# Performance work log

Measured on AMD Instinct MI355X. Metric: run time of the kernel, lower is better.

## Reference

```python
import jax, jax.numpy as jnp
import numpy as np

# ViT-Base config
C, H, W = 3, 224, 224
NP = 14            # n_patches per side
PS = 16            # patch size (H // NP)
IN_D = C * PS * PS # 768
D = 768            # hidden_d
NH = 12            # n_heads
DH = D // NH       # 64
L = 12             # n_blocks
MLP = 4 * D        # mlp_ratio * hidden_d
OUT = 1000         # out_d
B = 64             # batch
S = NP * NP + 1    # 197 tokens (cls + patches)
EPS = 1e-5


def _pos_embed(seq_len, d):
    # get_positional_embeddings: sin on even dims, cos on odd dims
    i = jnp.arange(seq_len, dtype=jnp.float32)[:, None]
    j = jnp.arange(d, dtype=jnp.float32)[None, :]
    angle = i / jnp.power(10000.0, (j - j % 2) / d)
    return jnp.where(j % 2 == 0, jnp.sin(angle), jnp.cos(angle))


def _ln(x, g, b):
    m = x.mean(-1, keepdims=True)
    v = ((x - m) ** 2).mean(-1, keepdims=True)
    return (x - m) * jax.lax.rsqrt(v + EPS) * g + b


def _attn(x, qkv_w, qkv_b, out_w, out_b):
    n, s, _ = x.shape
    qkv = (x @ qkv_w + qkv_b).reshape(n, s, NH, 3, DH)  # matches torch chunk layout
    q, k, v = qkv[..., 0, :], qkv[..., 1, :], qkv[..., 2, :]
    scores = jnp.einsum('bqhd,bkhd->bhqk', q, k) / (DH ** 0.5)
    w = jax.nn.softmax(scores, axis=-1)
    o = jnp.einsum('bhqk,bkhd->bqhd', w, v).reshape(n, s, D)
    return o @ out_w + out_b


def setup_inputs() -> dict:
    key = jax.random.key(0)
    ks = jax.random.split(key, 16)
    sd = 0.02
    return {
        'images': jax.random.normal(ks[0], (B, C, H, W), jnp.float32),
        'lm_w': jax.random.normal(ks[1], (IN_D, D), jnp.float32) * sd,
        'lm_b': jnp.zeros((D,), jnp.float32),
        'cls_tok': jax.random.uniform(ks[2], (1, D), jnp.float32),
        'ln1_g': jnp.ones((L, D), jnp.float32),
        'ln1_b': jnp.zeros((L, D), jnp.float32),
        'qkv_w': jax.random.normal(ks[3], (L, D, 3 * D), jnp.float32) * sd,
        'qkv_b': jnp.zeros((L, 3 * D), jnp.float32),
        'out_w': jax.random.normal(ks[4], (L, D, D), jnp.float32) * sd,
        'out_b': jnp.zeros((L, D), jnp.float32),
        'ln2_g': jnp.ones((L, D), jnp.float32),
        'ln2_b': jnp.zeros((L, D), jnp.float32),
        'mlp1_w': jax.random.normal(ks[5], (L, D, MLP), jnp.float32) * sd,
        'mlp1_b': jnp.zeros((L, MLP), jnp.float32),
        'mlp2_w': jax.random.normal(ks[6], (L, MLP, D), jnp.float32) * sd,
        'mlp2_b': jnp.zeros((L, D), jnp.float32),
        'head_w': jax.random.normal(ks[7], (D, OUT), jnp.float32) * sd,
        'head_b': jnp.zeros((OUT,), jnp.float32),
    }


def reference(images, lm_w, lm_b, cls_tok, ln1_g, ln1_b, qkv_w, qkv_b,
              out_w, out_b, ln2_g, ln2_b, mlp1_w, mlp1_b, mlp2_w, mlp2_b,
              head_w, head_b):
    n = images.shape[0]
    # patchify: (N,C,H,W) -> (N, NP*NP, C*PS*PS), per-patch flatten order (C, ph, pw)
    p = images.reshape(n, C, NP, PS, NP, PS).transpose(0, 2, 4, 1, 3, 5)
    p = p.reshape(n, NP * NP, IN_D)
    tok = p @ lm_w + lm_b                                   # (N, 196, D)
    cls = jnp.broadcast_to(cls_tok, (n, 1, D))
    x = jnp.concatenate([cls, tok], axis=1) + _pos_embed(S, D)
    for l in range(L):
        x = x + _attn(_ln(x, ln1_g[l], ln1_b[l]), qkv_w[l], qkv_b[l], out_w[l], out_b[l])
        h = _ln(x, ln2_g[l], ln2_b[l])
        x = x + (jax.nn.gelu(h @ mlp1_w[l] + mlp1_b[l], approximate=False) @ mlp2_w[l] + mlp2_b[l])
    return jax.nn.softmax(x[:, 0] @ head_w + head_b, axis=-1)
```

## Files before the change

### kernel.cpp

```cpp
#include <hip/hip_runtime.h>
#include <hip/hip_bf16.h>
#include <math.h>

#define WS_B 64
#define WS_S 197
#define WS_D 768
#define WS_NH 12
#define WS_L 12
#define WS_MLP 3072
#define WS_OUT 1000
#define WS_IND 768
#define WS_NPAT 196
#define SP 208
#define JP 224

typedef __attribute__((ext_vector_type(8))) short bf16x8;
typedef __attribute__((ext_vector_type(4))) float f32x4;

static __device__ __forceinline__ float bf2f(short s) {
    unsigned u = ((unsigned)(unsigned short)s) << 16;
    return __builtin_bit_cast(float, u);
}
static __device__ __forceinline__ short f2bf(float f) {
    unsigned u = __builtin_bit_cast(unsigned, f);
    u = (u + 0x7FFF + ((u >> 16) & 1)) >> 16;
    return (short)u;
}

__global__ __launch_bounds__(256) void wconv_kernel(
    const float* __restrict__ W, short* __restrict__ Wh, int K, int N)
{
    int idx = blockIdx.x * 256 + threadIdx.x;
    int total = (K >> 3) * N;
    if (idx >= total) return;
    int n = idx % N, k8 = idx / N, k0 = k8 << 3;
    short hi[8];
#pragma unroll
    for (int j = 0; j < 8; ++j) hi[j] = f2bf(W[(size_t)(k0 + j) * N + n]);
    *(bf16x8*)(Wh + (size_t)n * K + k0) = *(bf16x8*)hi;
}

__global__ __launch_bounds__(256) void mfma_gemm(
    const short* __restrict__ A, int lda,
    const short* __restrict__ Bh,
    const float* __restrict__ bias, const float* __restrict__ res,
    float* __restrict__ outF, short* __restrict__ outH, int ldc,
    int M, int N, int K, int act)
{
    __shared__ short As[128 * 64];
    __shared__ short Bs[128 * 64];

    const int tid = threadIdx.x;
    const int w = tid >> 6, lane = tid & 63;
    const int bm = blockIdx.y * 128, bn = blockIdx.x * 128;
    const int wm = (w >> 1) * 64, wn = (w & 1) * 64;
    const int lr = lane & 15, lq = lane >> 4;

    f32x4 acc[4][4];
#pragma unroll
    for (int i = 0; i < 4; ++i)
#pragma unroll
        for (int j = 0; j < 4; ++j) acc[i][j] = (f32x4){0.f, 0.f, 0.f, 0.f};

    int aoff[2][4], boff[2][4];
#pragma unroll
    for (int ks = 0; ks < 2; ++ks)
#pragma unroll
        for (int f = 0; f < 4; ++f) {
            int r = wm + f * 16 + lr;
            aoff[ks][f] = r * 64 + (((ks * 4 + lq) ^ (lr & 7)) << 3);
            int rn = wn + f * 16 + lr;
            boff[ks][f] = rn * 64 + (((ks * 4 + lq) ^ (lr & 7)) << 3);
        }

    int srow[4], scs[4];
#pragma unroll
    for (int i = 0; i < 4; ++i) {
        int chunk = w * 64 + i * 256 + lane;
        int row = chunk >> 3, c = chunk & 7;
        srow[i] = row;
        scs[i] = c ^ (row & 7);
    }

    for (int k0 = 0; k0 < K; k0 += 64) {
#pragma unroll
        for (int i = 0; i < 4; ++i) {
            int ldsbase = (w * 64 + i * 256) * 8;
            int arow = bm + srow[i]; if (arow >= M) arow = M - 1;
            const short* ga = A + (size_t)arow * lda + k0 + scs[i] * 8;
            __builtin_amdgcn_global_load_lds(
                (const __attribute__((address_space(1))) void*)ga,
                (__attribute__((address_space(3))) void*)(As + ldsbase), 16, 0, 0);
            const short* gh = Bh + (size_t)(bn + srow[i]) * K + k0 + scs[i] * 8;
            __builtin_amdgcn_global_load_lds(
                (const __attribute__((address_space(1))) void*)gh,
                (__attribute__((address_space(3))) void*)(Bs + ldsbase), 16, 0, 0);
        }
        asm volatile("s_waitcnt vmcnt(0)" ::: "memory");
        __syncthreads();

#pragma unroll
        for (int ks = 0; ks < 2; ++ks) {
            bf16x8 av[4], bv[4];
#pragma unroll
            for (int f = 0; f < 4; ++f) av[f] = *(const bf16x8*)&As[aoff[ks][f]];
#pragma unroll
            for (int f = 0; f < 4; ++f) bv[f] = *(const bf16x8*)&Bs[boff[ks][f]];
#pragma unroll
            for (int fm = 0; fm < 4; ++fm)
#pragma unroll
                for (int fn = 0; fn < 4; ++fn)
                    acc[fm][fn] = __builtin_amdgcn_mfma_f32_16x16x32_bf16(
                        av[fm], bv[fn], acc[fm][fn], 0, 0, 0);
        }
        __syncthreads();
    }

#pragma unroll
    for (int fm = 0; fm < 4; ++fm)
#pragma unroll
        for (int fn = 0; fn < 4; ++fn) {
            int gc = bn + wn + fn * 16 + lr;
            float bvs = bias ? bias[gc] : 0.f;
            int grb = bm + wm + fm * 16 + lq * 4;
#pragma unroll
            for (int r = 0; r < 4; ++r) {
                int gr = grb + r;
                if (gr >= M) continue;
                float v = acc[fm][fn][r] + bvs;
                if (act == 1) v = 0.5f * v * (1.f + erff(v * 0.70710678118654752440f));
                if (res) v += res[(size_t)gr * ldc + gc];
                if (outF) outF[(size_t)gr * ldc + gc] = v;
                else      outH[(size_t)gr * ldc + gc] = f2bf(v);
            }
        }
}

__global__ __launch_bounds__(256) void attn_kernel(
    const short* __restrict__ qkv, short* __restrict__ o)
{
    __shared__ short Qs[SP * 64];
    __shared__ short Ks[SP * 64];
    __shared__ short Vt[64 * 256];
    __shared__ short Ps[4][16 * 256];

    const int bh = blockIdx.x;
    const int n = bh / WS_NH, h = bh % WS_NH;
    const short* base = qkv + (size_t)n * WS_S * 2304 + h * 192;
    const int tid = threadIdx.x;
    const int w = tid >> 6, lane = tid & 63;
    const int lr = lane & 15, lq = lane >> 4;

    const bf16x8 z8 = {0, 0, 0, 0, 0, 0, 0, 0};
    for (int i = lane; i < 512; i += 64) *(bf16x8*)&Ps[w][i * 8] = z8;

    for (int u = tid; u < SP * 8; u += 256) {
        int row = u >> 3, c = u & 7;
        int cs = c ^ (row & 7);
        bf16x8 vq = z8, vk = z8;
        if (row < WS_S) {
            const short* rp = base + (size_t)row * 2304;
            vq = *(const bf16x8*)(rp + cs * 8);
            vk = *(const bf16x8*)(rp + 64 + cs * 8);
        }
        *(bf16x8*)&Qs[row * 64 + c * 8] = vq;
        *(bf16x8*)&Ks[row * 64 + c * 8] = vk;
    }

    for (int u = tid; u < 64 * (JP / 2); u += 256) {
        int d = u & 63, jp = u >> 6;
        int j = jp * 2;
        unsigned val = 0;
        if (j < WS_S) {
            unsigned lo = (unsigned short)base[(size_t)j * 2304 + 128 + d];
            unsigned hi = (j + 1 < WS_S) ? (unsigned short)base[(size_t)(j + 1) * 2304 + 128 + d] : 0u;
            val = lo | (hi << 16);
        }
        int cj = j >> 3, e = j & 7;
        *(unsigned*)&Vt[d * 256 + ((cj ^ (d & 7)) << 3) + e] = val;
    }
    __syncthreads();

    for (int qt = w; qt < 13; qt += 4) {
        bf16x8 qv[2];
#pragma unroll
        for (int ks = 0; ks < 2; ++ks)
            qv[ks] = *(const bf16x8*)&Qs[(qt * 16 + lr) * 64 + (((ks * 4 + lq) ^ (lr & 7)) << 3)];
        f32x4 acc[13];
#pragma unroll
        for (int jt = 0; jt < 13; ++jt) acc[jt] = (f32x4){0.f, 0.f, 0.f, 0.f};
#pragma unroll
        for (int jt = 0; jt < 13; ++jt)
#pragma unroll
            for (int ks = 0; ks < 2; ++ks) {
                bf16x8 kv = *(const bf16x8*)&Ks[(jt * 16 + lr) * 64 + (((ks * 4 + lq) ^ (lr & 7)) << 3)];
                acc[jt] = __builtin_amdgcn_mfma_f32_16x16x32_bf16(kv, qv[ks], acc[jt], 0, 0, 0);
            }

        float s[13][4];
        float m = -1e30f;
#pragma unroll
        for (int jt = 0; jt < 13; ++jt)
#pragma unroll
            for (int r = 0; r < 4; ++r) {
                int j = jt * 16 + lq * 4 + r;
                float v = acc[jt][r] * 0.125f;
                s[jt][r] = v;
                if (j < WS_S) m = fmaxf(m, v);
            }
        m = fmaxf(m, __shfl_xor(m, 16));
        m = fmaxf(m, __shfl_xor(m, 32));
        float sum = 0.f;
#pragma unroll
        for (int jt = 0; jt < 13; ++jt)
#pragma unroll
            for (int r = 0; r < 4; ++r) {
                int j = jt * 16 + lq * 4 + r;
                float e = (j < WS_S) ? __expf(s[jt][r] - m) : 0.f;
                s[jt][r] = e;
                sum += e;
            }
        sum += __shfl_xor(sum, 16);
        sum += __shfl_xor(sum, 32);
        float inv = (sum > 0.f) ? 1.f / sum : 0.f;

#pragma unroll
        for (int jt = 0; jt < 13; ++jt) {
            int jb = jt * 16 + lq * 4;
            int cj = jb >> 3, e = jb & 7;
            int off = lr * 256 + ((cj ^ (lr & 7)) << 3) + e;
            unsigned p01 = (unsigned)(unsigned short)f2bf(s[jt][0] * inv) |
                           ((unsigned)(unsigned short)f2bf(s[jt][1] * inv) << 16);
            unsigned p23 = (unsigned)(unsigned short)f2bf(s[jt][2] * inv) |
                           ((unsigned)(unsigned short)f2bf(s[jt][3] * inv) << 16);
            *(unsigned*)&Ps[w][off] = p01;
            *(unsigned*)&Ps[w][off + 2] = p23;
        }

        bf16x8 pa[7];
#pragma unroll
        for (int ks = 0; ks < 7; ++ks)
            pa[ks] = *(const bf16x8*)&Ps[w][lr * 256 + (((ks * 4 + lq) ^ (lr & 7)) << 3)];
#pragma unroll
        for (int dt = 0; dt < 4; ++dt) {
            f32x4 oacc = (f32x4){0.f, 0.f, 0.f, 0.f};
#pragma unroll
            for (int ks = 0; ks < 7; ++ks) {
                bf16x8 vb = *(const bf16x8*)&Vt[(dt * 16 + lr) * 256 + (((ks * 4 + lq) ^ (lr & 7)) << 3)];
                oacc = __builtin_amdgcn_mfma_f32_16x16x32_bf16(pa[ks], vb, oacc, 0, 0, 0);
            }
#pragma unroll
            for (int r = 0; r < 4; ++r) {
                int qg = qt * 16 + lq * 4 + r;
                if (qg < WS_S)
                    o[((size_t)n * WS_S + qg) * WS_D + h * 64 + dt * 16 + lr] = f2bf(oacc[r]);
            }
        }
    }
}

__global__ __launch_bounds__(256) void gemm_kernel(
    const float* __restrict__ A, int lda,
    const float* __restrict__ B, int ldb,
    const float* __restrict__ bias,
    float* __restrict__ C, int ldc,
    int M, int N, int K)
{
    __shared__ float As[16][128];
    __shared__ float Bs[16][128];
    const int tid = threadIdx.x;
    const int tx = tid & 15, ty = tid >> 4;
    const int bm = blockIdx.y * 128, bn = blockIdx.x * 128;
    float acc[8][8];
#pragma unroll
    for (int i = 0; i < 8; ++i)
#pragma unroll
        for (int j = 0; j < 8; ++j) acc[i][j] = 0.f;
    const int arow = tid >> 2, acol4 = (tid & 3) << 2;
    const int brow = tid >> 5, bcol4 = (tid & 31) << 2;
    for (int k0 = 0; k0 < K; k0 += 16) {
#pragma unroll
        for (int r = 0; r < 2; ++r) {
            int m = bm + arow + r * 64;
            int k = k0 + acol4;
            float4 v = make_float4(0.f, 0.f, 0.f, 0.f);
            if (m < M) {
                const float* ap = A + (size_t)m * lda + k;
                if (k + 3 < K) v = *(const float4*)ap;
                else { if (k < K) v.x = ap[0]; if (k + 1 < K) v.y = ap[1]; if (k + 2 < K) v.z = ap[2]; }
            }
            As[acol4 + 0][arow + r * 64] = v.x;
            As[acol4 + 1][arow + r * 64] = v.y;
            As[acol4 + 2][arow + r * 64] = v.z;
            As[acol4 + 3][arow + r * 64] = v.w;
        }
#pragma unroll
        for (int r = 0; r < 2; ++r) {
            int k = k0 + brow + r * 8;
            int nn = bn + bcol4;
            float4 v = make_float4(0.f, 0.f, 0.f, 0.f);
            if (k < K) {
                const float* bp = B + (size_t)k * ldb + nn;
                if (nn + 3 < N) v = *(const float4*)bp;
                else { if (nn < N) v.x = bp[0]; if (nn + 1 < N) v.y = bp[1]; if (nn + 2 < N) v.z = bp[2]; }
            }
            *(float4*)&Bs[brow + r * 8][bcol4] = v;
        }
        __syncthreads();
#pragma unroll
        for (int kk = 0; kk < 16; ++kk) {
            float4 a0 = *(const float4*)&As[kk][ty * 4];
            float4 a1 = *(const float4*)&As[kk][64 + ty * 4];
            float4 b0 = *(const float4*)&Bs[kk][tx * 4];
            float4 b1 = *(const float4*)&Bs[kk][64 + tx * 4];
            float a[8] = {a0.x, a0.y, a0.z, a0.w, a1.x, a1.y, a1.z, a1.w};
            float b[8] = {b0.x, b0.y, b0.z, b0.w, b1.x, b1.y, b1.z, b1.w};
#pragma unroll
            for (int i = 0; i < 8; ++i)
#pragma unroll
                for (int j = 0; j < 8; ++j) acc[i][j] += a[i] * b[j];
        }
        __syncthreads();
    }
#pragma unroll
    for (int i = 0; i < 8; ++i) {
        int m = bm + ((i < 4) ? (ty * 4 + i) : (64 + ty * 4 + i - 4));
        if (m >= M) continue;
#pragma unroll
        for (int j = 0; j < 8; ++j) {
            int nn = bn + ((j < 4) ? (tx * 4 + j) : (64 + tx * 4 + j - 4));
            if (nn >= N) continue;
            C[(size_t)m * ldc + nn] = acc[i][j] + (bias ? bias[nn] : 0.f);
        }
    }
}

__global__ __launch_bounds__(256) void ln_kernel(
    const float* __restrict__ x, const float* __restrict__ g,
    const float* __restrict__ b, short* __restrict__ y)
{
    __shared__ float ssum[4], ssq[4];
    const int row = blockIdx.x;
    const int tid = threadIdx.x;
    const float* xr = x + (size_t)row * WS_D;
    float v0 = xr[tid], v1 = xr[tid + 256], v2 = xr[tid + 512];
    float s = v0 + v1 + v2;
    float q = v0 * v0 + v1 * v1 + v2 * v2;
#pragma unroll
    for (int off = 32; off > 0; off >>= 1) {
        s += __shfl_xor(s, off);
        q += __shfl_xor(q, off);
    }
    if ((tid & 63) == 0) { ssum[tid >> 6] = s; ssq[tid >> 6] = q; }
    __syncthreads();
    s = ssum[0] + ssum[1] + ssum[2] + ssum[3];
    q = ssq[0] + ssq[1] + ssq[2] + ssq[3];
    const float mean = s * (1.f / WS_D);
    const float var = q * (1.f / WS_D) - mean * mean;
    const float rstd = rsqrtf(var + 1e-5f);
    short* yr = y + (size_t)row * WS_D;
    yr[tid]       = f2bf((v0 - mean) * rstd * g[tid]       + b[tid]);
    yr[tid + 256] = f2bf((v1 - mean) * rstd * g[tid + 256] + b[tid + 256]);
    yr[tid + 512] = f2bf((v2 - mean) * rstd * g[tid + 512] + b[tid + 512]);
}

__global__ void pe_kernel(float* __restrict__ pe)
{
    int idx = blockIdx.x * 256 + threadIdx.x;
    if (idx >= WS_S * WS_D) return;
    int s = idx / WS_D, j = idx % WS_D;
    float expo = (float)(j & ~1) / (float)WS_D;
    float angle = (float)s * powf(10000.f, -expo);
    pe[idx] = (j & 1) ? cosf(angle) : sinf(angle);
}

__global__ void patchify_kernel(const float* __restrict__ img, short* __restrict__ p)
{
    int idx = blockIdx.x * 256 + threadIdx.x;
    const int total = WS_B * WS_NPAT * WS_IND;
    if (idx >= total) return;
    int pid = idx / WS_IND;
    int e = idx % WS_IND;
    int n = pid / WS_NPAT, patch = pid % WS_NPAT;
    int c = e >> 8, r = e & 255;
    int iy = r >> 4, ix = r & 15;
    int py = patch / 14, px = patch % 14;
    p[idx] = f2bf(img[(((size_t)n * 3 + c) * 224 + py * 16 + iy) * 224 + px * 16 + ix]);
}

__global__ void assemble_kernel(const float* __restrict__ tok, const float* __restrict__ cls,
                                const float* __restrict__ pe, float* __restrict__ x)
{
    int idx = blockIdx.x * 256 + threadIdx.x;
    const int total = WS_B * WS_S * WS_D;
    if (idx >= total) return;
    int row = idx / WS_D, d = idx % WS_D;
    int n = row / WS_S, s = row % WS_S;
    float v = (s == 0) ? cls[d] : tok[((size_t)n * WS_NPAT + (s - 1)) * WS_D + d];
    x[idx] = v + pe[s * WS_D + d];
}

__global__ __launch_bounds__(256) void softmax1000_kernel(
    const float* __restrict__ logits, float* __restrict__ out)
{
    __shared__ float rmax[4], rsum[4];
    const int row = blockIdx.x;
    const int tid = threadIdx.x;
    const float* lr = logits + (size_t)row * WS_OUT;
    float v[4];
    float mx = -INFINITY;
#pragma unroll
    for (int i = 0; i < 4; ++i) {
        int c = tid + i * 256;
        v[i] = (c < WS_OUT) ? lr[c] : -INFINITY;
        mx = fmaxf(mx, v[i]);
    }
#pragma unroll
    for (int off = 32; off > 0; off >>= 1) mx = fmaxf(mx, __shfl_xor(mx, off));
    if ((tid & 63) == 0) rmax[tid >> 6] = mx;
    __syncthreads();
    mx = fmaxf(fmaxf(rmax[0], rmax[1]), fmaxf(rmax[2], rmax[3]));
    float sum = 0.f;
#pragma unroll
    for (int i = 0; i < 4; ++i) {
        int c = tid + i * 256;
        v[i] = (c < WS_OUT) ? expf(v[i] - mx) : 0.f;
        sum += v[i];
    }
#pragma unroll
    for (int off = 32; off > 0; off >>= 1) sum += __shfl_xor(sum, off);
    if ((tid & 63) == 0) rsum[tid >> 6] = sum;
    __syncthreads();
    sum = rsum[0] + rsum[1] + rsum[2] + rsum[3];
    const float inv = 1.f / sum;
#pragma unroll
    for (int i = 0; i < 4; ++i) {
        int c = tid + i * 256;
        if (c < WS_OUT) out[(size_t)row * WS_OUT + c] = v[i] * inv;
    }
}

extern "C" void kernel_launch(void* const* d_in, const int* in_sizes, int n_in,
                              void* d_out, int out_size, void* d_ws, size_t ws_size,
                              hipStream_t stream)
{
    const float* images = (const float*)d_in[0];
    const float* lm_w   = (const float*)d_in[1];
    const float* lm_b   = (const float*)d_in[2];
    const float* cls    = (const float*)d_in[3];
    const float* ln1_g  = (const float*)d_in[4];
    const float* ln1_b  = (const float*)d_in[5];
    const float* qkv_w  = (const float*)d_in[6];
    const float* qkv_b  = (const float*)d_in[7];
    const float* out_w  = (const float*)d_in[8];
    const float* out_b  = (const float*)d_in[9];
    const float* ln2_g  = (const float*)d_in[10];
    const float* ln2_b  = (const float*)d_in[11];
    const float* mlp1_w = (const float*)d_in[12];
    const float* mlp1_b = (const float*)d_in[13];
    const float* mlp2_w = (const float*)d_in[14];
    const float* mlp2_b = (const float*)d_in[15];
    const float* head_w = (const float*)d_in[16];
    const float* head_b = (const float*)d_in[17];

    const int ROWS = WS_B * WS_S;
    char* wsb = (char*)d_ws;
    size_t off = 0;
    auto alloc = [&](size_t bytes) {
        void* p = wsb + off;
        off += (bytes + 255) & ~(size_t)255;
        return p;
    };
    float* pe     = (float*)alloc((size_t)WS_S * WS_D * 4);
    float* x      = (float*)alloc((size_t)ROWS * WS_D * 4);
    short* xh     = (short*)alloc((size_t)ROWS * WS_D * 2);
    short* qkvh   = (short*)alloc((size_t)ROWS * 2304 * 2);
    short* oh     = (short*)alloc((size_t)ROWS * WS_D * 2);
    short* hh     = (short*)alloc((size_t)ROWS * WS_MLP * 2);
    float* logits = (float*)alloc((size_t)WS_B * WS_OUT * 4);
    short* ph     = (short*)alloc((size_t)WS_B * WS_NPAT * WS_IND * 2);
    short* qWh  = (short*)alloc((size_t)WS_D * 2304 * 2);
    short* oWh  = (short*)alloc((size_t)WS_D * WS_D * 2);
    short* m1Wh = (short*)alloc((size_t)WS_D * WS_MLP * 2);
    short* m2Wh = (short*)alloc((size_t)WS_MLP * WS_D * 2);
    short* lmWh = (short*)alloc((size_t)WS_IND * WS_D * 2);
    float* tok  = (float*)hh;

    pe_kernel<<<(WS_S * WS_D + 255) / 256, 256, 0, stream>>>(pe);
    patchify_kernel<<<(WS_B * WS_NPAT * WS_IND + 255) / 256, 256, 0, stream>>>(images, ph);
    wconv_kernel<<<(WS_IND / 8 * WS_D + 255) / 256, 256, 0, stream>>>(lm_w, lmWh, WS_IND, WS_D);
    mfma_gemm<<<dim3(6, 98), 256, 0, stream>>>(
        ph, WS_IND, lmWh, lm_b, nullptr, tok, nullptr, WS_D,
        WS_B * WS_NPAT, WS_D, WS_IND, 0);
    assemble_kernel<<<(WS_B * WS_S * WS_D + 255) / 256, 256, 0, stream>>>(tok, cls, pe, x);

    for (int l = 0; l < WS_L; ++l) {
        wconv_kernel<<<(WS_D / 8 * 2304 + 255) / 256, 256, 0, stream>>>(
            qkv_w + (size_t)l * WS_D * 2304, qWh, WS_D, 2304);
        wconv_kernel<<<(WS_D / 8 * WS_D + 255) / 256, 256, 0, stream>>>(
            out_w + (size_t)l * WS_D * WS_D, oWh, WS_D, WS_D);
        wconv_kernel<<<(WS_D / 8 * WS_MLP + 255) / 256, 256, 0, stream>>>(
            mlp1_w + (size_t)l * WS_D * WS_MLP, m1Wh, WS_D, WS_MLP);
        wconv_kernel<<<(WS_MLP / 8 * WS_D + 255) / 256, 256, 0, stream>>>(
            mlp2_w + (size_t)l * WS_MLP * WS_D, m2Wh, WS_MLP, WS_D);

        ln_kernel<<<ROWS, 256, 0, stream>>>(x, ln1_g + l * WS_D, ln1_b + l * WS_D, xh);
        mfma_gemm<<<dim3(18, 99), 256, 0, stream>>>(
            xh, WS_D, qWh, qkv_b + l * 2304, nullptr, nullptr, qkvh, 2304,
            ROWS, 2304, WS_D, 0);
        attn_kernel<<<WS_B * WS_NH, 256, 0, stream>>>(qkvh, oh);
        mfma_gemm<<<dim3(6, 99), 256, 0, stream>>>(
            oh, WS_D, oWh, out_b + l * WS_D, x, x, nullptr, WS_D,
            ROWS, WS_D, WS_D, 0);
        ln_kernel<<<ROWS, 256, 0, stream>>>(x, ln2_g + l * WS_D, ln2_b + l * WS_D, xh);
        mfma_gemm<<<dim3(24, 99), 256, 0, stream>>>(
            xh, WS_D, m1Wh, mlp1_b + l * WS_MLP, nullptr, nullptr, hh, WS_MLP,
            ROWS, WS_MLP, WS_D, 1);
        mfma_gemm<<<dim3(6, 99), 256, 0, stream>>>(
            hh, WS_MLP, m2Wh, mlp2_b + l * WS_D, x, x, nullptr, WS_D,
            ROWS, WS_D, WS_MLP, 0);
    }

    gemm_kernel<<<dim3(8, 1), 256, 0, stream>>>(
        x, WS_S * WS_D, head_w, WS_OUT, head_b, logits, WS_OUT,
        WS_B, WS_OUT, WS_D);
    softmax1000_kernel<<<WS_B, 256, 0, stream>>>(logits, (float*)d_out);
}
```

Measured before the change: 6.266 ms.

## Remap GEMM workgroups across XCDs, vectorize V transpose, simplify head GEMM

The MFMA GEMM now remaps its linear workgroup index so that consecutive tiles land on the same XCD, which is meant to improve L2 reuse of shared A/B tiles. The attention kernel loads V rows with 16-byte vector loads and scatters them into the transposed LDS layout, replacing the old per-element strided global loads. A waitcnt is added before the P tile is read back from LDS. The tiled fp32 head GEMM is replaced by a simple per-output dot-product kernel that launches more blocks but has no data reuse.

```diff
diff --git a/kernel.cpp b/kernel.cpp
--- a/kernel.cpp
+++ b/kernel.cpp
@@ -27,6 +27,12 @@
     return (short)u;
 }
 
+static __device__ __forceinline__ int xcd_remap(int wg, int nwg) {
+    int q = nwg >> 3, r = nwg & 7;
+    int xcd = wg & 7, idx = wg >> 3;
+    return (xcd < r ? xcd * (q + 1) : r * (q + 1) + (xcd - r) * q) + idx;
+}
+
 __global__ __launch_bounds__(256) void wconv_kernel(
     const float* __restrict__ W, short* __restrict__ Wh, int K, int N)
 {
@@ -52,7 +58,10 @@
 
     const int tid = threadIdx.x;
     const int w = tid >> 6, lane = tid & 63;
-    const int bm = blockIdx.y * 128, bn = blockIdx.x * 128;
+    const int nwg = gridDim.x * gridDim.y;
+    int wg = blockIdx.y * gridDim.x + blockIdx.x;
+    wg = xcd_remap(wg, nwg);
+    const int bm = (wg / gridDim.x) * 128, bn = (wg % gridDim.x) * 128;
     const int wm = (w >> 1) * 64, wn = (w & 1) * 64;
     const int lr = lane & 15, lq = lane >> 4;
 
@@ -167,17 +176,17 @@
         *(bf16x8*)&Ks[row * 64 + c * 8] = vk;
     }
 
-    for (int u = tid; u < 64 * (JP / 2); u += 256) {
-        int d = u & 63, jp = u >> 6;
-        int j = jp * 2;
-        unsigned val = 0;
-        if (j < WS_S) {
-            unsigned lo = (unsigned short)base[(size_t)j * 2304 + 128 + d];
-            unsigned hi = (j + 1 < WS_S) ? (unsigned short)base[(size_t)(j + 1) * 2304 + 128 + d] : 0u;
-            val = lo | (hi << 16);
-        }
-        int cj = j >> 3, e = j & 7;
-        *(unsigned*)&Vt[d * 256 + ((cj ^ (d & 7)) << 3) + e] = val;
+#pragma unroll
+    for (int pass = 0; pass < 7; ++pass) {
+        int r = pass * 32 + (tid >> 3);
+        int c = tid & 7;
+        bf16x8 v = z8;
+        if (r < WS_S) v = *(const bf16x8*)(base + (size_t)r * 2304 + 128 + c * 8);
+#pragma unroll
+        for (int e = 0; e < 8; ++e) {
+            int d = c * 8 + e;
+            Vt[d * 256 + ((((r >> 3)) ^ (d & 7)) << 3) + (r & 7)] = v[e];
+        }
     }
     __syncthreads();
 
@@ -236,6 +245,7 @@
             *(unsigned*)&Ps[w][off] = p01;
             *(unsigned*)&Ps[w][off + 2] = p23;
         }
+        __builtin_amdgcn_s_waitcnt(0);
 
         bf16x8 pa[7];
 #pragma unroll
@@ -259,80 +269,18 @@
     }
 }
 
-__global__ __launch_bounds__(256) void gemm_kernel(
-    const float* __restrict__ A, int lda,
-    const float* __restrict__ B, int ldb,
-    const float* __restrict__ bias,
-    float* __restrict__ C, int ldc,
-    int M, int N, int K)
-{
-    __shared__ float As[16][128];
-    __shared__ float Bs[16][128];
-    const int tid = threadIdx.x;
-    const int tx = tid & 15, ty = tid >> 4;
-    const int bm = blockIdx.y * 128, bn = blockIdx.x * 128;
-    float acc[8][8];
-#pragma unroll
-    for (int i = 0; i < 8; ++i)
-#pragma unroll
-        for (int j = 0; j < 8; ++j) acc[i][j] = 0.f;
-    const int arow = tid >> 2, acol4 = (tid & 3) << 2;
-    const int brow = tid >> 5, bcol4 = (tid & 31) << 2;
-    for (int k0 = 0; k0 < K; k0 += 16) {
-#pragma unroll
-        for (int r = 0; r < 2; ++r) {
-            int m = bm + arow + r * 64;
-            int k = k0 + acol4;
-            float4 v = make_float4(0.f, 0.f, 0.f, 0.f);
-            if (m < M) {
-                const float* ap = A + (size_t)m * lda + k;
-                if (k + 3 < K) v = *(const float4*)ap;
-                else { if (k < K) v.x = ap[0]; if (k + 1 < K) v.y = ap[1]; if (k + 2 < K) v.z = ap[2]; }
-            }
-            As[acol4 + 0][arow + r * 64] = v.x;
-            As[acol4 + 1][arow + r * 64] = v.y;
-            As[acol4 + 2][arow + r * 64] = v.z;
-            As[acol4 + 3][arow + r * 64] = v.w;
-        }
-#pragma unroll
-        for (int r = 0; r < 2; ++r) {
-            int k = k0 + brow + r * 8;
-            int nn = bn + bcol4;
-            float4 v = make_float4(0.f, 0.f, 0.f, 0.f);
-            if (k < K) {
-                const float* bp = B + (size_t)k * ldb + nn;
-                if (nn + 3 < N) v = *(const float4*)bp;
-                else { if (nn < N) v.x = bp[0]; if (nn + 1 < N) v.y = bp[1]; if (nn + 2 < N) v.z = bp[2]; }
-            }
-            *(float4*)&Bs[brow + r * 8][bcol4] = v;
-        }
-        __syncthreads();
-#pragma unroll
-        for (int kk = 0; kk < 16; ++kk) {
-            float4 a0 = *(const float4*)&As[kk][ty * 4];
-            float4 a1 = *(const float4*)&As[kk][64 + ty * 4];
-            float4 b0 = *(const float4*)&Bs[kk][tx * 4];
-            float4 b1 = *(const float4*)&Bs[kk][64 + tx * 4];
-            float a[8] = {a0.x, a0.y, a0.z, a0.w, a1.x, a1.y, a1.z, a1.w};
-            float b[8] = {b0.x, b0.y, b0.z, b0.w, b1.x, b1.y, b1.z, b1.w};
-#pragma unroll
-            for (int i = 0; i < 8; ++i)
-#pragma unroll
-                for (int j = 0; j < 8; ++j) acc[i][j] += a[i] * b[j];
-        }
-        __syncthreads();
-    }
-#pragma unroll
-    for (int i = 0; i < 8; ++i) {
-        int m = bm + ((i < 4) ? (ty * 4 + i) : (64 + ty * 4 + i - 4));
-        if (m >= M) continue;
-#pragma unroll
-        for (int j = 0; j < 8; ++j) {
-            int nn = bn + ((j < 4) ? (tx * 4 + j) : (64 + tx * 4 + j - 4));
-            if (nn >= N) continue;
-            C[(size_t)m * ldc + nn] = acc[i][j] + (bias ? bias[nn] : 0.f);
-        }
-    }
+__global__ __launch_bounds__(256) void head_kernel(
+    const float* __restrict__ x, const float* __restrict__ W,
+    const float* __restrict__ bias, float* __restrict__ out)
+{
+    int c = blockIdx.x * 16 + (threadIdx.x & 15);
+    int m = blockIdx.y * 16 + (threadIdx.x >> 4);
+    if (c >= WS_OUT) return;
+    const float* xr = x + (size_t)m * (WS_S * WS_D);
+    float acc = bias[c];
+    for (int k = 0; k < WS_D; ++k)
+        acc = fmaf(xr[k], W[(size_t)k * WS_OUT + c], acc);
+    out[(size_t)m * WS_OUT + c] = acc;
 }
 
 __global__ __launch_bounds__(256) void ln_kernel(
@@ -521,8 +469,6 @@
             ROWS, WS_D, WS_MLP, 0);
     }
 
-    gemm_kernel<<<dim3(8, 1), 256, 0, stream>>>(
-        x, WS_S * WS_D, head_w, WS_OUT, head_b, logits, WS_OUT,
-        WS_B, WS_OUT, WS_D);
+    head_kernel<<<dim3((WS_OUT + 15) / 16, 4), 256, 0, stream>>>(x, head_w, head_b, logits);
     softmax1000_kernel<<<WS_B, 256, 0, stream>>>(logits, (float*)d_out);
 }
```

Result: faster. 5.841 ms (-6.8%).
